# Performance work log

Measured on AMD Instinct MI355X. Metric: run time of the kernel, lower is better.

Reference implementation:

```python
import jax, jax.numpy as jnp
import numpy as np

N_NODES = 100      # fixed: actor_fc expects 6000 = 100 * 60
IN_C    = 65536    # chev_conv_state_dim
OUT_C   = 60
K       = 3        # Chebyshev order
ACTION  = 100
N_EDGES = 1600


def setup_inputs() -> dict:
    key = jax.random.key(0)
    ks = jax.random.split(key, 20)
    s = 0.02  # small init scale
    f32 = jnp.float32
    return {
        "substrate_features": jax.random.normal(ks[0], (N_NODES, IN_C), f32),
        "substrate_edge_index": jax.random.randint(ks[1], (2, N_EDGES), 0, N_NODES),
        "vnr_features": jax.random.uniform(ks[2], (1, 3), f32),
        # ChebConv params: weight [K, IN_C, OUT_C], bias [OUT_C]
        "actor_cheb_w": (jax.random.normal(ks[3], (K, IN_C, OUT_C), f32) * s),
        "actor_cheb_b": jnp.zeros((OUT_C,), f32),
        "critic_cheb_w": (jax.random.normal(ks[4], (K, IN_C, OUT_C), f32) * s),
        "critic_cheb_b": jnp.zeros((OUT_C,), f32),
        # three Linear(1,60) per head, stacked: w [3, 60], b [3, 60]
        "actor_vnr_w": jax.random.normal(ks[5], (3, OUT_C), f32) * s,
        "actor_vnr_b": jnp.zeros((3, OUT_C), f32),
        "critic_vnr_w": jax.random.normal(ks[6], (3, OUT_C), f32) * s,
        "critic_vnr_b": jnp.zeros((3, OUT_C), f32),
        # heads
        "actor_fc_w": jax.random.normal(ks[7], (N_NODES * OUT_C, ACTION), f32) * s,
        "actor_fc_b": jnp.zeros((ACTION,), f32),
        "critic_fc_w": jax.random.normal(ks[8], (N_NODES * OUT_C, 1), f32) * s,
        "critic_fc_b": jnp.zeros((1,), f32),
    }


def _cheb_conv(x, src, dst, W, b):
    """PyG ChebConv with sym normalization, lambda_max=2 => L_hat = -D^-1/2 A D^-1/2.
    Z0 = x, Z1 = L_hat x, Z2 = 2 L_hat Z1 - Z0; out = sum_k Zk @ W[k] + b."""
    n = x.shape[0]
    ones = jnp.ones(src.shape[0], x.dtype)
    deg = jax.ops.segment_sum(ones, src, num_segments=n)
    dinv = jnp.where(deg > 0, jax.lax.rsqrt(jnp.maximum(deg, 1.0)), 0.0)
    w_norm = -dinv[src] * dinv[dst]  # [E]

    def lhat(z):  # sparse propagate: gather src rows, scale, scatter-add at dst
        return jax.ops.segment_sum(w_norm[:, None] * z[src], dst, num_segments=n)

    z0 = x
    z1 = lhat(z0)
    z2 = 2.0 * lhat(z1) - z0
    return z0 @ W[0] + z1 @ W[1] + z2 @ W[2] + b


def _vnr_sum(v, w, b):
    # sum of three Linear(1,60) outputs on scalars v[0], v[1], v[2] -> [60]
    return (v[:, None] * w + b).sum(axis=0)


def reference(substrate_features, substrate_edge_index, vnr_features,
              actor_cheb_w, actor_cheb_b, critic_cheb_w, critic_cheb_b,
              actor_vnr_w, actor_vnr_b, critic_vnr_w, critic_vnr_b,
              actor_fc_w, actor_fc_b, critic_fc_w, critic_fc_b):
    src, dst = substrate_edge_index[0], substrate_edge_index[1]
    v = vnr_features[0]  # [3]

    emb_a = jnp.tanh(_cheb_conv(substrate_features, src, dst, actor_cheb_w, actor_cheb_b))
    emb_a = emb_a + _vnr_sum(v, actor_vnr_w, actor_vnr_b)  # broadcast [N,60] + [60]
    flat_a = emb_a.reshape(1, -1)  # [1, 6000]
    logits = flat_a @ actor_fc_w + actor_fc_b  # [1, ACTION]

    emb_c = jnp.tanh(_cheb_conv(substrate_features, src, dst, critic_cheb_w, critic_cheb_b))
    emb_c = emb_c + _vnr_sum(v, critic_vnr_w, critic_vnr_b)
    flat_c = emb_c.reshape(1, -1)
    values = flat_c @ critic_fc_w + critic_fc_b  # [1, 1]

    return logits, values
```

## Files before the change

kernel.cpp:

```cpp
#include <hip/hip_runtime.h>
#include <math.h>

#define KDIM    65536
#define NNODES  100
#define OUTC    60
#define YW      64
#define YSLAB   (NNODES*YW)

#define BK5     64
#define ITERS5  16
#define SLAB5   (BK5*ITERS5)
#define NKC5    (KDIM/SLAB5)
#define CHUNK   256
#define NKC     256
#define STEPS   (CHUNK/32)

#define WS_Y    10048
#define WS_E    48448
#define XB_OFF_BYTES   245760ull
#define XB_BYTES       (100ull*65536ull*2ull)
#define WS_NEED_BYTES  (XB_OFF_BYTES + XB_BYTES)

typedef short bf16x8 __attribute__((ext_vector_type(8)));
typedef float f32x4  __attribute__((ext_vector_type(4)));
typedef unsigned short ushort8 __attribute__((ext_vector_type(8)));

__device__ inline unsigned short f2bf(float f) {
    union { float f; unsigned u; } x; x.f = f;
    unsigned r = x.u + 0x7FFFu + ((x.u >> 16) & 1u);
    return (unsigned short)(r >> 16);
}

__global__ __launch_bounds__(256) void k_cvt_x(const float* __restrict__ x,
                                               ushort8* __restrict__ xb,
                                               float* __restrict__ Y) {
    int g = blockIdx.x * 256 + threadIdx.x;
    if (g < 9600) ((f32x4*)Y)[g] = (f32x4){};
    for (int i = g; i < 819200; i += 204800) {
        const float4 lo = ((const float4*)x)[2 * i];
        const float4 hi = ((const float4*)x)[2 * i + 1];
        ushort8 o;
        o[0] = f2bf(lo.x); o[1] = f2bf(lo.y); o[2] = f2bf(lo.z); o[3] = f2bf(lo.w);
        o[4] = f2bf(hi.x); o[5] = f2bf(hi.y); o[6] = f2bf(hi.z); o[7] = f2bf(hi.w);
        xb[i] = o;
    }
}

__global__ __launch_bounds__(256) void k_gemm7(const unsigned short* __restrict__ xb,
                                               const float* __restrict__ wa,
                                               const float* __restrict__ wc,
                                               float* __restrict__ Y) {
    __shared__ unsigned short Ab[2][14 * 512];
    __shared__ unsigned short padlds[512];
    const int b    = blockIdx.x;
    const int lo8  = b & 7, q = b >> 3;
    const int hk   = q % 6;
    const int kc   = lo8 + 8 * (q / 6);
    const int wave = threadIdx.x >> 6;
    const int lane = threadIdx.x & 63;
    const int n16  = lane & 15;
    const int quad = lane >> 4;
    const int c0   = wave * 16;
    const int cidx = min(c0 + n16, OUTC - 1);
    const int kb0  = kc * SLAB5;

    const float* Wg = (hk < 3 ? wa : wc) + (size_t)(hk % 3) * ((size_t)KDIM * OUTC);

    auto DMA = [&](int buf, int kb) {
#pragma unroll
        for (int j5 = 0; j5 < 4; ++j5) {
            int j = wave + j5 * 4;
            int chunk = j * 64 + lane;
            int m  = chunk >> 3;
            int cc = (chunk & 7) ^ (m & 7);
            const unsigned short* src =
                xb + (size_t)min(m, NNODES - 1) * KDIM + kb + cc * 8;
            void* dst = (j < 14) ? (void*)&Ab[buf][j * 512] : (void*)padlds;
            __builtin_amdgcn_global_load_lds(
                (const __attribute__((address_space(1))) void*)src,
                (__attribute__((address_space(3))) void*)dst, 16, 0, 0);
        }
    };

    float breg[2][16];
    auto LOADB = [&](int pb, int kb) {
        const float* base = Wg + (size_t)(kb + quad * 8) * OUTC + cidx;
#pragma unroll
        for (int s = 0; s < 2; ++s)
#pragma unroll
            for (int j = 0; j < 8; ++j)
                breg[pb][s * 8 + j] = base[(s * 32 + j) * OUTC];
    };

    DMA(0, kb0);
    LOADB(0, kb0);
    f32x4 acc[7] = {};

#pragma unroll
    for (int it = 0; it < ITERS5; ++it) {
        if (it + 1 < ITERS5) {
            DMA((it + 1) & 1, kb0 + (it + 1) * BK5);
            LOADB((it + 1) & 1, kb0 + (it + 1) * BK5);
            asm volatile("s_waitcnt vmcnt(20)" ::: "memory");
        } else {
            asm volatile("s_waitcnt vmcnt(0)" ::: "memory");
        }
        __builtin_amdgcn_s_barrier();
        const unsigned short* A = Ab[it & 1];
#pragma unroll
        for (int s = 0; s < 2; ++s) {
            bf16x8 bfr;
#pragma unroll
            for (int j = 0; j < 8; ++j)
                bfr[j] = (short)f2bf(breg[it & 1][s * 8 + j]);
            int ch = (s * 4 + quad) ^ (n16 & 7);
#pragma unroll
            for (int t = 0; t < 7; ++t) {
                bf16x8 afr = *(const bf16x8*)(A + (t * 16 + n16) * BK5 + ch * 8);
                acc[t] = __builtin_amdgcn_mfma_f32_16x16x32_bf16(afr, bfr, acc[t], 0, 0, 0);
            }
        }
        __builtin_amdgcn_s_barrier();
    }

    float* Yb = Y + hk * YSLAB;
#pragma unroll
    for (int t = 0; t < 7; ++t)
#pragma unroll
        for (int r = 0; r < 4; ++r) {
            int row = t * 16 + quad * 4 + r;
            if (row < NNODES)
                atomicAdd(&Yb[row * YW + c0 + n16], acc[t][r]);
        }
}

__global__ __launch_bounds__(256, 2) void k_gemm_f32(const float* __restrict__ x,
                                                     const float* __restrict__ wa,
                                                     const float* __restrict__ wc,
                                                     float* __restrict__ Y) {
    const int hk   = blockIdx.x;
    const int kc   = blockIdx.y;
    const int wave = threadIdx.x >> 6;
    const int lane = threadIdx.x & 63;
    const int n16  = lane & 15;
    const int quad = lane >> 4;
    const float* W = (hk < 3 ? wa : wc) + (size_t)(hk % 3) * ((size_t)KDIM * OUTC);
    const int c0   = wave * 16;
    const int cidx = min(c0 + n16, OUTC - 1);
    const int kb0  = kc * CHUNK + quad * 8;
    const float* ap[7];
#pragma unroll
    for (int t = 0; t < 7; ++t)
        ap[t] = x + (size_t)min(n16 + 16 * t, NNODES - 1) * KDIM + kb0;
    const float* bp = W + (size_t)kb0 * OUTC + cidx;
    f32x4 acc[7] = {};
#pragma unroll 2
    for (int s = 0; s < STEPS; ++s) {
        bf16x8 bfr;
        const float* qq = bp + (size_t)s * 32 * OUTC;
#pragma unroll
        for (int j = 0; j < 8; ++j) bfr[j] = (short)f2bf(qq[j * OUTC]);
#pragma unroll
        for (int t = 0; t < 7; ++t) {
            const float* p = ap[t] + s * 32;
            float4 lo = *(const float4*)p;
            float4 hi = *(const float4*)(p + 4);
            bf16x8 afr;
            afr[0] = (short)f2bf(lo.x); afr[1] = (short)f2bf(lo.y);
            afr[2] = (short)f2bf(lo.z); afr[3] = (short)f2bf(lo.w);
            afr[4] = (short)f2bf(hi.x); afr[5] = (short)f2bf(hi.y);
            afr[6] = (short)f2bf(hi.z); afr[7] = (short)f2bf(hi.w);
            acc[t] = __builtin_amdgcn_mfma_f32_16x16x32_bf16(afr, bfr, acc[t], 0, 0, 0);
        }
    }
    float* Yb = Y + hk * YSLAB;
#pragma unroll
    for (int t = 0; t < 7; ++t)
#pragma unroll
        for (int r = 0; r < 4; ++r) {
            int row = t * 16 + quad * 4 + r;
            if (row < NNODES)
                atomicAdd(&Yb[row * YW + c0 + n16], acc[t][r]);
        }
}

__global__ __launch_bounds__(128) void k_emb(const int* __restrict__ ei,
                                             const float* __restrict__ Y,
                                             const float* __restrict__ vnr,
                                             const float* __restrict__ avw,
                                             const float* __restrict__ avb,
                                             const float* __restrict__ cvw,
                                             const float* __restrict__ cvb,
                                             const float* __restrict__ acb,
                                             const float* __restrict__ ccb,
                                             const float* __restrict__ afcb,
                                             const float* __restrict__ cfcb,
                                             float* __restrict__ E,
                                             float* __restrict__ out) {
    __shared__ float Sp[NNODES * 101];
    __shared__ float y0[NNODES], y1[NNODES], y2[NNODES], t2[NNODES];
    __shared__ int   deg[NNODES];
    __shared__ float dinv[NNODES];
    const int b = blockIdx.x, head = b / OUTC, c = b % OUTC;
    const int t = threadIdx.x;
    const int* src = ei;
    const int* dst = ei + 1600;

    for (int i = t; i < NNODES * 101; i += 128) Sp[i] = 0.f;
    if (t < NNODES) deg[t] = 0;
    __syncthreads();
    for (int e = t; e < 1600; e += 128) atomicAdd(&deg[src[e]], 1);
    __syncthreads();
    if (t < NNODES) { int d = deg[t]; dinv[t] = (d > 0) ? rsqrtf((float)d) : 0.f; }
    __syncthreads();
    for (int e = t; e < 1600; e += 128) {
        int s = src[e], d = dst[e];
        atomicAdd(&Sp[d * 101 + s], -dinv[s] * dinv[d]);
    }
    const float* Yh = Y + (size_t)head * 3 * YSLAB;
    if (t < NNODES) {
        y0[t] = Yh[t * YW + c];
        y1[t] = Yh[YSLAB + t * YW + c];
        y2[t] = Yh[2 * YSLAB + t * YW + c];
    }
    if (b == 0 && t < 101) out[t] = (t < 100) ? afcb[t] : cfcb[0];
    __syncthreads();

    float z1 = 0.f, s2 = 0.f;
    if (t < NNODES) {
        const float* sr = Sp + t * 101;
        for (int m = 0; m < NNODES; ++m) { z1 += sr[m] * y1[m]; s2 += sr[m] * y2[m]; }
        t2[t] = s2;
    }
    __syncthreads();
    if (t < NNODES) {
        const float* sr = Sp + t * 101;
        float t3 = 0.f;
        for (int m = 0; m < NNODES; ++m) t3 += sr[m] * t2[m];
        const float* cb = head ? ccb : acb;
        const float* vw = head ? cvw : avw;
        const float* vb = head ? cvb : avb;
        float u  = y0[t] + z1 + 2.f * t3 - y2[t] + cb[c];
        float vs = vnr[0] * vw[c]        + vb[c]
                 + vnr[1] * vw[OUTC + c] + vb[OUTC + c]
                 + vnr[2] * vw[2*OUTC+c] + vb[2*OUTC+c];
        E[head * (NNODES * OUTC) + t * OUTC + c] = tanhf(u) + vs;
    }
}

__global__ __launch_bounds__(128) void k_heads(const float* __restrict__ E,
                                               const float* __restrict__ afw,
                                               const float* __restrict__ cfw,
                                               float* __restrict__ out) {
    __shared__ float ea[25], ec[25];
    const int b = blockIdx.x, t = threadIdx.x;
    const int f0 = b * 25;
    if (t < 25) {
        ea[t] = E[f0 + t];
        ec[t] = E[NNODES * OUTC + f0 + t];
    }
    __syncthreads();
    if (t < 100) {
        float s = 0.f;
#pragma unroll
        for (int i = 0; i < 25; ++i) s += ea[i] * afw[(size_t)(f0 + i) * 100 + t];
        atomicAdd(&out[t], s);
    } else if (t == 100) {
        float s = 0.f;
#pragma unroll
        for (int i = 0; i < 25; ++i) s += ec[i] * cfw[f0 + i];
        atomicAdd(&out[100], s);
    }
}

extern "C" void kernel_launch(void* const* d_in, const int* in_sizes, int n_in,
                              void* d_out, int out_size, void* d_ws, size_t ws_size,
                              hipStream_t stream) {
    const float* x    = (const float*)d_in[0];
    const int*   ei   = (const int*)  d_in[1];
    const float* vnr  = (const float*)d_in[2];
    const float* wa   = (const float*)d_in[3];
    const float* acb  = (const float*)d_in[4];
    const float* wc   = (const float*)d_in[5];
    const float* ccb  = (const float*)d_in[6];
    const float* avw  = (const float*)d_in[7];
    const float* avb  = (const float*)d_in[8];
    const float* cvw  = (const float*)d_in[9];
    const float* cvb  = (const float*)d_in[10];
    const float* afw  = (const float*)d_in[11];
    const float* afcb = (const float*)d_in[12];
    const float* cfw  = (const float*)d_in[13];
    const float* cfcb = (const float*)d_in[14];

    float* ws = (float*)d_ws;
    float* Y  = ws + WS_Y;
    float* E  = ws + WS_E;
    float* out = (float*)d_out;

    if (ws_size >= WS_NEED_BYTES) {
        unsigned short* xb = (unsigned short*)((char*)d_ws + XB_OFF_BYTES);
        k_cvt_x<<<800, 256, 0, stream>>>(x, (ushort8*)xb, Y);
        k_gemm7<<<384, 256, 0, stream>>>(xb, wa, wc, Y);
    } else {
        hipMemsetAsync((char*)d_ws + WS_Y * 4, 0, (WS_E - WS_Y) * 4, stream);
        k_gemm_f32<<<dim3(6, NKC), 256, 0, stream>>>(x, wa, wc, Y);
    }

    k_emb<<<120, 128, 0, stream>>>(ei, Y, vnr, avw, avb, cvw, cvb,
                                   acb, ccb, afcb, cfcb, E, out);
    k_heads<<<240, 128, 0, stream>>>(E, afw, cfw, out);
}
```

Before: 204.4 us.

## Fuse FC heads into embedding kernel and halve GEMM K-slab for more blocks

Merges the separate heads kernel into the embedding kernel, so each (head, channel) block computes its node embeddings and atomically adds its partial FC contributions straight into the output. This drops one launch and the round trip of the intermediate embedding buffer. Output zeroing moves into the conversion kernel (or a memset on the fallback path). The GEMM slab per block is halved and the grid doubled to 768 blocks for more parallelism, at the cost of twice as many atomic adds into Y.

```diff
diff --git a/kernel.cpp b/kernel.cpp
--- a/kernel.cpp
+++ b/kernel.cpp
@@ -8,7 +8,7 @@
 #define YSLAB   (NNODES*YW)
 
 #define BK5     64
-#define ITERS5  16
+#define ITERS5  8
 #define SLAB5   (BK5*ITERS5)
 #define NKC5    (KDIM/SLAB5)
 #define CHUNK   256
@@ -33,9 +33,11 @@
 
 __global__ __launch_bounds__(256) void k_cvt_x(const float* __restrict__ x,
                                                ushort8* __restrict__ xb,
-                                               float* __restrict__ Y) {
+                                               float* __restrict__ Y,
+                                               float* __restrict__ out) {
     int g = blockIdx.x * 256 + threadIdx.x;
     if (g < 9600) ((f32x4*)Y)[g] = (f32x4){};
+    if (g < 101)  out[g] = 0.f;
     for (int i = g; i < 819200; i += 204800) {
         const float4 lo = ((const float4*)x)[2 * i];
         const float4 hi = ((const float4*)x)[2 * i + 1];
@@ -46,7 +48,7 @@
     }
 }
 
-__global__ __launch_bounds__(256) void k_gemm7(const unsigned short* __restrict__ xb,
+__global__ __launch_bounds__(256) void k_gemm8(const unsigned short* __restrict__ xb,
                                                const float* __restrict__ wa,
                                                const float* __restrict__ wc,
                                                float* __restrict__ Y) {
@@ -184,21 +186,23 @@
         }
 }
 
-__global__ __launch_bounds__(128) void k_emb(const int* __restrict__ ei,
-                                             const float* __restrict__ Y,
-                                             const float* __restrict__ vnr,
-                                             const float* __restrict__ avw,
-                                             const float* __restrict__ avb,
-                                             const float* __restrict__ cvw,
-                                             const float* __restrict__ cvb,
-                                             const float* __restrict__ acb,
-                                             const float* __restrict__ ccb,
-                                             const float* __restrict__ afcb,
-                                             const float* __restrict__ cfcb,
-                                             float* __restrict__ E,
-                                             float* __restrict__ out) {
+__global__ __launch_bounds__(128) void k_embh(const int* __restrict__ ei,
+                                              const float* __restrict__ Y,
+                                              const float* __restrict__ vnr,
+                                              const float* __restrict__ avw,
+                                              const float* __restrict__ avb,
+                                              const float* __restrict__ cvw,
+                                              const float* __restrict__ cvb,
+                                              const float* __restrict__ acb,
+                                              const float* __restrict__ ccb,
+                                              const float* __restrict__ afcb,
+                                              const float* __restrict__ cfcb,
+                                              const float* __restrict__ afw,
+                                              const float* __restrict__ cfw,
+                                              float* __restrict__ out) {
     __shared__ float Sp[NNODES * 101];
     __shared__ float y0[NNODES], y1[NNODES], y2[NNODES], t2[NNODES];
+    __shared__ float e[NNODES];
     __shared__ int   deg[NNODES];
     __shared__ float dinv[NNODES];
     const int b = blockIdx.x, head = b / OUTC, c = b % OUTC;
@@ -209,12 +213,12 @@
     for (int i = t; i < NNODES * 101; i += 128) Sp[i] = 0.f;
     if (t < NNODES) deg[t] = 0;
     __syncthreads();
-    for (int e = t; e < 1600; e += 128) atomicAdd(&deg[src[e]], 1);
+    for (int ed = t; ed < 1600; ed += 128) atomicAdd(&deg[src[ed]], 1);
     __syncthreads();
     if (t < NNODES) { int d = deg[t]; dinv[t] = (d > 0) ? rsqrtf((float)d) : 0.f; }
     __syncthreads();
-    for (int e = t; e < 1600; e += 128) {
-        int s = src[e], d = dst[e];
+    for (int ed = t; ed < 1600; ed += 128) {
+        int s = src[ed], d = dst[ed];
         atomicAdd(&Sp[d * 101 + s], -dinv[s] * dinv[d]);
     }
     const float* Yh = Y + (size_t)head * 3 * YSLAB;
@@ -223,7 +227,6 @@
         y1[t] = Yh[YSLAB + t * YW + c];
         y2[t] = Yh[2 * YSLAB + t * YW + c];
     }
-    if (b == 0 && t < 101) out[t] = (t < 100) ? afcb[t] : cfcb[0];
     __syncthreads();
 
     float z1 = 0.f, s2 = 0.f;
@@ -233,6 +236,7 @@
         t2[t] = s2;
     }
     __syncthreads();
+    float ev = 0.f;
     if (t < NNODES) {
         const float* sr = Sp + t * 101;
         float t3 = 0.f;
@@ -244,32 +248,27 @@
         float vs = vnr[0] * vw[c]        + vb[c]
                  + vnr[1] * vw[OUTC + c] + vb[OUTC + c]
                  + vnr[2] * vw[2*OUTC+c] + vb[2*OUTC+c];
-        E[head * (NNODES * OUTC) + t * OUTC + c] = tanhf(u) + vs;
-    }
-}
-
-__global__ __launch_bounds__(128) void k_heads(const float* __restrict__ E,
-                                               const float* __restrict__ afw,
-                                               const float* __restrict__ cfw,
-                                               float* __restrict__ out) {
-    __shared__ float ea[25], ec[25];
-    const int b = blockIdx.x, t = threadIdx.x;
-    const int f0 = b * 25;
-    if (t < 25) {
-        ea[t] = E[f0 + t];
-        ec[t] = E[NNODES * OUTC + f0 + t];
-    }
-    __syncthreads();
-    if (t < 100) {
-        float s = 0.f;
-#pragma unroll
-        for (int i = 0; i < 25; ++i) s += ea[i] * afw[(size_t)(f0 + i) * 100 + t];
-        atomicAdd(&out[t], s);
-    } else if (t == 100) {
-        float s = 0.f;
-#pragma unroll
-        for (int i = 0; i < 25; ++i) s += ec[i] * cfw[f0 + i];
-        atomicAdd(&out[100], s);
+        ev = tanhf(u) + vs;
+        e[t] = ev;
+    }
+    __syncthreads();
+
+    if (head == 0) {
+        if (t < NNODES) {
+            float s = (c == 0) ? afcb[t] : 0.f;
+            const float* wrow = afw + (size_t)c * 100 + t;
+#pragma unroll 4
+            for (int n = 0; n < NNODES; ++n) s += e[n] * wrow[(size_t)n * 6000];
+            atomicAdd(&out[t], s);
+        }
+    } else {
+        float p = (t < NNODES) ? ev * cfw[t * OUTC + c] : 0.f;
+#pragma unroll
+        for (int off = 32; off > 0; off >>= 1) p += __shfl_down(p, off, 64);
+        __shared__ float wsum[2];
+        if ((t & 63) == 0) wsum[t >> 6] = p;
+        __syncthreads();
+        if (t == 0) atomicAdd(&out[100], wsum[0] + wsum[1] + (c == 0 ? cfcb[0] : 0.f));
     }
 }
 
@@ -294,19 +293,18 @@
 
     float* ws = (float*)d_ws;
     float* Y  = ws + WS_Y;
-    float* E  = ws + WS_E;
     float* out = (float*)d_out;
 
     if (ws_size >= WS_NEED_BYTES) {
         unsigned short* xb = (unsigned short*)((char*)d_ws + XB_OFF_BYTES);
-        k_cvt_x<<<800, 256, 0, stream>>>(x, (ushort8*)xb, Y);
-        k_gemm7<<<384, 256, 0, stream>>>(xb, wa, wc, Y);
+        k_cvt_x<<<800, 256, 0, stream>>>(x, (ushort8*)xb, Y, out);
+        k_gemm8<<<768, 256, 0, stream>>>(xb, wa, wc, Y);
     } else {
         hipMemsetAsync((char*)d_ws + WS_Y * 4, 0, (WS_E - WS_Y) * 4, stream);
+        hipMemsetAsync(d_out, 0, 101 * sizeof(float), stream);
         k_gemm_f32<<<dim3(6, NKC), 256, 0, stream>>>(x, wa, wc, Y);
     }
 
-    k_emb<<<120, 128, 0, stream>>>(ei, Y, vnr, avw, avb, cvw, cvb,
-                                   acb, ccb, afcb, cfcb, E, out);
-    k_heads<<<240, 128, 0, stream>>>(E, afw, cfw, out);
-}
+    k_embh<<<120, 128, 0, stream>>>(ei, Y, vnr, avw, avb, cvw, cvb,
+                                    acb, ccb, afcb, cfcb, afw, cfw, out);
+}
```

After: 205.5 us. No clear change (+0.5%).
